# Kernel optimization log

Measured on AMD Instinct MI355X. Metric: run time of the kernel, lower is better.

The kernel has to match this reference:

```python
import jax, jax.numpy as jnp
import numpy as np

B = 65536      # batch of pose frames
FD = 267       # frame_dim
NC = 1         # num_condition_frames
NF = 1         # num_future_predictions
H = 256        # hidden_size
L = 64         # latent_size
K = 1024       # num_embeddings


def setup_inputs() -> dict:
    ks = jax.random.split(jax.random.key(0), 16)
    def W(k, o, i):
        return (jax.random.normal(k, (o, i), jnp.float32) * (1.0 / np.sqrt(i))).astype(jnp.float32)
    return {
        "x": jax.random.normal(ks[0], (B, FD * NF), jnp.float32),
        "c": jax.random.normal(ks[1], (B, FD * NC), jnp.float32),
        "fc1_w": W(ks[2], H, FD * (NF + NC)), "fc1_b": jnp.zeros((H,), jnp.float32),
        "fc2_w": W(ks[3], H, H), "fc2_b": jnp.zeros((H,), jnp.float32),
        "fc3_w": W(ks[4], H, H), "fc3_b": jnp.zeros((H,), jnp.float32),
        "mu_w": W(ks[5], L, H), "mu_b": jnp.zeros((L,), jnp.float32),
        "fc4_w": W(ks[6], H, L + FD * NC), "fc4_b": jnp.zeros((H,), jnp.float32),
        "fc5_w": W(ks[7], H, H), "fc5_b": jnp.zeros((H,), jnp.float32),
        "fc6_w": W(ks[8], H, H), "fc6_b": jnp.zeros((H,), jnp.float32),
        "out_w": W(ks[9], NF * FD, H), "out_b": jnp.zeros((NF * FD,), jnp.float32),
        "embed": jax.random.normal(ks[10], (L, K), jnp.float32),  # codebook [latent, num_embeddings]
    }


def reference(x, c, fc1_w, fc1_b, fc2_w, fc2_b, fc3_w, fc3_b, mu_w, mu_b,
              fc4_w, fc4_b, fc5_w, fc5_b, fc6_w, fc6_b, out_w, out_b, embed):
    relu = jax.nn.relu
    # encode
    s = jnp.concatenate([x, c], axis=1)                      # [B, FD*(NF+NC)]
    h = relu(s @ fc1_w.T + fc1_b)
    h = relu(h @ fc2_w.T + fc2_b)
    h = relu(h @ fc3_w.T + fc3_b)
    mu = h @ mu_w.T + mu_b                                   # [B, L]
    # vector quantizer (eval mode: no EMA buffer updates; outputs identical)
    dist = (jnp.sum(mu * mu, axis=1, keepdims=True)
            - 2.0 * (mu @ embed)
            + jnp.sum(embed * embed, axis=0, keepdims=True))  # [B, K]
    idx = jnp.argmax(-dist, axis=1)                           # [B]
    onehot = jax.nn.one_hot(idx, K, dtype=mu.dtype)           # [B, K]
    quantize = jnp.take(embed.T, idx, axis=0)                 # [B, L] codebook gather
    loss = jnp.mean((jax.lax.stop_gradient(quantize) - mu) ** 2)
    q_st = mu + jax.lax.stop_gradient(quantize - mu)          # straight-through
    avg_probs = jnp.mean(onehot, axis=0)
    perplexity = jnp.exp(-jnp.sum(avg_probs * jnp.log(avg_probs + 1e-10)))
    # decode
    s2 = jnp.concatenate([q_st, c], axis=1)                   # [B, L + FD*NC]
    h = relu(s2 @ fc4_w.T + fc4_b)
    h = relu(h @ fc5_w.T + fc5_b)
    h = relu(h @ fc6_w.T + fc6_b)
    recon = h @ out_w.T + out_b                               # [B, NF*FD]
    return recon, loss, perplexity
```

## Files before the change

kernel.cpp:

```cpp
#include <hip/hip_runtime.h>


using short8 = __attribute__((ext_vector_type(8))) short;
using f32x4  = __attribute__((ext_vector_type(4))) float;
using f32x16 = __attribute__((ext_vector_type(16))) float;

#define USHORT unsigned short
#define UINT   unsigned int

#define PS_W1  139264
#define PS_W2  65536
#define PS_MU  16384
#define PS_WE  65536

#define STRF 260
#define STRA 360
#define STRB 264

static const size_t OFF_COUNTS = 262144;
static const size_t OFF_LOSS   = 266240;
static const size_t OFF_ENORM  = 266304;
static const size_t OFF_W1     = 270400;
static const size_t OFF_W2     = 1105984;
static const size_t OFF_W3     = 1499200;
static const size_t OFF_WMU    = 1892416;
static const size_t OFF_WE     = 1990720;
static const size_t OFF_W4     = 2383936;
static const size_t OFF_W5     = 2564160;
static const size_t OFF_W6     = 2695232;
static const size_t OFF_WO     = 2826304;

__device__ __forceinline__ float b2f(USHORT u){
  return __uint_as_float(((UINT)u) << 16);
}
__device__ __forceinline__ USHORT f2b(float f){
  UINT u = __float_as_uint(f);
  u += 0x7fffu + ((u >> 16) & 1u);
  return (USHORT)(u >> 16);
}
__device__ __forceinline__ float loadF(const void* p, long i, int f32m){
  if (f32m) return ((const float*)p)[i];
  return b2f(((const USHORT*)p)[i]);
}
__device__ __forceinline__ void split3(float h, USHORT& a, USHORT& b, USHORT& c){
  a = f2b(h); float r = h - b2f(a);
  b = f2b(r); r -= b2f(b);
  c = f2b(r);
}
__device__ __forceinline__ void splitT(float h, USHORT& a, USHORT& b, USHORT& c){
  UINT u = __float_as_uint(h);
  a = (USHORT)(u >> 16);
  float r = h - __uint_as_float(u & 0xffff0000u);
  UINT v = __float_as_uint(r);
  b = (USHORT)(v >> 16);
  float r2 = r - __uint_as_float(v & 0xffff0000u);
  c = f2b(r2);
}
__device__ __forceinline__ f32x4 mfma16(short8 a, short8 b, f32x4 c){
  return __builtin_amdgcn_mfma_f32_16x16x32_bf16(a, b, c, 0, 0, 0);
}
__device__ __forceinline__ f32x16 mfma32(short8 a, short8 b, f32x16 c){
  return __builtin_amdgcn_mfma_f32_32x32x16_bf16(a, b, c, 0, 0, 0);
}
__device__ __forceinline__ void zero16(f32x16& v){
  #pragma unroll
  for (int i = 0; i < 16; ++i) v[i] = 0.f;
}
__device__ __forceinline__ void splitAT(const float* p, short8& A0, short8& A1, short8& A2){
  #pragma unroll
  for (int j = 0; j < 8; ++j){
    USHORT t0, t1, t2; splitT(p[j], t0, t1, t2);
    A0[j] = (short)t0; A1[j] = (short)t1; A2[j] = (short)t2;
  }
}
__device__ __forceinline__ int detect_f32(const void* x){
  UINT u = ((const UINT*)x)[threadIdx.x & 63];
  int e = (int)((u >> 7) & 0xFFu);
  unsigned long long m = __ballot(e >= 117 && e <= 130);
  return __popcll(m) < 32;
}

__device__ __forceinline__ void fillW(USHORT* dst, const void* src,
                                      int Kpad, int N, int Ksrc, int Nsrc,
                                      int srcStride, bool kmajor, int t,
                                      int f32m, int planes)
{
  int total = Kpad * N;
  if (t >= total) return;
  int j = t & 7, rest = t >> 3;
  int n = rest % N, kg = rest / N;
  int k = kg*8 + j;
  float v = 0.f;
  if (k < Ksrc && n < Nsrc)
    v = loadF(src, kmajor ? (long)k*srcStride + n : (long)n*srcStride + k, f32m);
  if (planes == 1){ dst[t] = f2b(v); return; }
  USHORT t0, t1, t2; split3(v, t0, t1, t2);
  dst[t] = t0; dst[total + t] = t1; dst[2*total + t] = t2;
}

__global__ void vq_prep_kernel(
    const void* xx,
    const void* fc1w, const void* fc2w, const void* fc3w,
    const void* muw,  const void* fc4w, const void* fc5w,
    const void* fc6w, const void* outw, const void* embed,
    USHORT* W1p, USHORT* W2p, USHORT* W3p, USHORT* Wmup, USHORT* Wep,
    USHORT* W4p, USHORT* W5p, USHORT* W6p, USHORT* Wop,
    float* enorm, UINT* counts, float* loss_sum)
{
  int f32m = detect_f32(xx);
  int t = blockIdx.x * 256 + threadIdx.x;
  switch (blockIdx.y){
    case 0: fillW(W1p,  fc1w, 544, 256, 534, 256, 534, false, t, f32m, 3); break;
    case 1: fillW(W2p,  fc2w, 256, 256, 256, 256, 256, false, t, f32m, 3); break;
    case 2: fillW(W3p,  fc3w, 256, 256, 256, 256, 256, false, t, f32m, 3); break;
    case 3: fillW(Wmup, muw,  256,  64, 256,  64, 256, false, t, f32m, 3); break;
    case 4: fillW(Wep,  embed, 64, 1024, 64, 1024, 1024, true, t, f32m, 3); break;
    case 5: fillW(W4p,  fc4w, 352, 256, 331, 256, 331, false, t, f32m, 1); break;
    case 6: fillW(W5p,  fc5w, 256, 256, 256, 256, 256, false, t, f32m, 1); break;
    case 7: fillW(W6p,  fc6w, 256, 256, 256, 256, 256, false, t, f32m, 1); break;
    case 8: fillW(Wop,  outw, 256, 288, 256, 267, 256, false, t, f32m, 1); break;
    case 9:
      if (t < 1024){
        double s = 0.0;
        for (int l = 0; l < 64; ++l){
          double e = (double)loadF(embed, (long)l*1024 + t, f32m); s += e*e;
        }
        enorm[t] = (float)s;
      }
      break;
    case 10:
      if (t < 1024) counts[t] = 0u;
      if (t == 1024) *loss_sum = 0.f;
      break;
  }
}

__global__ __launch_bounds__(256, 4) void vq_main_kernel(
    const void* __restrict__ x,  const void* __restrict__ cc,
    const void* __restrict__ b1, const void* __restrict__ b2,
    const void* __restrict__ b3, const void* __restrict__ bmu,
    const void* __restrict__ b4, const void* __restrict__ b5,
    const void* __restrict__ b6, const void* __restrict__ bo,
    const void* __restrict__ embed,
    const USHORT* __restrict__ W1p, const USHORT* __restrict__ W2p,
    const USHORT* __restrict__ W3p, const USHORT* __restrict__ Wmup,
    const USHORT* __restrict__ Wep, const float* __restrict__ enorm,
    const USHORT* __restrict__ W4p, const USHORT* __restrict__ W5p,
    const USHORT* __restrict__ W6p, const USHORT* __restrict__ Wop,
    UINT* __restrict__ counts, float* __restrict__ loss_sum,
    void* __restrict__ out)
{
  __shared__ __align__(16) char U[39936];
  __shared__ float rMin[4][32];
  __shared__ int   rCode[4][32];
  float*  sF = (float*)U;
  USHORT* sA = (USHORT*)U;
  USHORT* sB = (USHORT*)(U + 23040);

  const int f32m = detect_f32(x);
  const int tid  = threadIdx.x;
  const int w    = tid >> 6;
  const int lane = tid & 63;
  const int hi   = lane >> 5;
  const int nn   = lane & 31;
  const int quad = lane >> 4;
  const int l16  = lane & 15;
  const int tb0  = w * 64;
  const long gbase = (long)blockIdx.x * 32;
  const long gr    = gbase + nn;

  f32x16 acc0, acc1;
  zero16(acc0); zero16(acc1);

  for (int ks = 0; ks < 34; ++ks){
    short8 A0, A1, A2;
    if (f32m){
      #pragma unroll
      for (int j = 0; j < 8; ++j){
        int col = ks*16 + hi*8 + j;
        float v = 0.f;
        if (col < 267)      v = ((const float*)x)[gr*267 + col];
        else if (col < 534) v = ((const float*)cc)[gr*267 + (col - 267)];
        USHORT t0, t1, t2; splitT(v, t0, t1, t2);
        A0[j] = (short)t0; A1[j] = (short)t1; A2[j] = (short)t2;
      }
    } else {
      #pragma unroll
      for (int j = 0; j < 8; ++j){
        int col = ks*16 + hi*8 + j;
        USHORT u = 0;
        if (col < 267)      u = ((const USHORT*)x)[gr*267 + col];
        else if (col < 534) u = ((const USHORT*)cc)[gr*267 + (col - 267)];
        A0[j] = (short)u;
      }
    }
    const USHORT* bp = W1p + (((ks*2 + hi)*256) + tb0 + nn)*8;
    short8 B00 = *(const short8*)bp;
    short8 B01 = *(const short8*)(bp + 256);
    if (!f32m){
      acc0 = mfma32(A0, B00, acc0); acc1 = mfma32(A0, B01, acc1);
    } else {
      short8 B10 = *(const short8*)(bp + PS_W1);
      short8 B11 = *(const short8*)(bp + PS_W1 + 256);
      short8 B20 = *(const short8*)(bp + 2*PS_W1);
      short8 B21 = *(const short8*)(bp + 2*PS_W1 + 256);
      acc0 = mfma32(A0, B00, acc0); acc1 = mfma32(A0, B01, acc1);
      acc0 = mfma32(A1, B00, acc0); acc1 = mfma32(A1, B01, acc1);
      acc0 = mfma32(A2, B00, acc0); acc1 = mfma32(A2, B01, acc1);
      acc0 = mfma32(A0, B10, acc0); acc1 = mfma32(A0, B11, acc1);
      acc0 = mfma32(A1, B10, acc0); acc1 = mfma32(A1, B11, acc1);
      acc0 = mfma32(A0, B20, acc0); acc1 = mfma32(A0, B21, acc1);
    }
  }
  {
    float bs0 = loadF(b1, tb0 + nn, f32m);
    float bs1 = loadF(b1, tb0 + 32 + nn, f32m);
    #pragma unroll
    for (int reg = 0; reg < 16; ++reg){
      int r = (reg&3) + 8*(reg>>2) + 4*hi;
      sF[r*STRF + tb0 + nn]      = fmaxf(acc0[reg] + bs0, 0.f);
      sF[r*STRF + tb0 + 32 + nn] = fmaxf(acc1[reg] + bs1, 0.f);
    }
  }
  __syncthreads();

  for (int layer = 0; layer < 2; ++layer){
    const USHORT* Wp = layer ? W3p : W2p;
    const void*   bb = layer ? (const void*)b3 : (const void*)b2;
    zero16(acc0); zero16(acc1);
    #pragma unroll 2
    for (int ks = 0; ks < 16; ++ks){
      short8 A0, A1, A2;
      splitAT(&sF[nn*STRF + ks*16 + hi*8], A0, A1, A2);
      const USHORT* bp = Wp + (((ks*2 + hi)*256) + tb0 + nn)*8;
      short8 B00 = *(const short8*)bp;
      short8 B01 = *(const short8*)(bp + 256);
      acc0 = mfma32(A0, B00, acc0); acc1 = mfma32(A0, B01, acc1);
      acc0 = mfma32(A1, B00, acc0); acc1 = mfma32(A1, B01, acc1);
      acc0 = mfma32(A2, B00, acc0); acc1 = mfma32(A2, B01, acc1);
      if (f32m){
        short8 B10 = *(const short8*)(bp + PS_W2);
        short8 B11 = *(const short8*)(bp + PS_W2 + 256);
        short8 B20 = *(const short8*)(bp + 2*PS_W2);
        short8 B21 = *(const short8*)(bp + 2*PS_W2 + 256);
        acc0 = mfma32(A0, B10, acc0); acc1 = mfma32(A0, B11, acc1);
        acc0 = mfma32(A1, B10, acc0); acc1 = mfma32(A1, B11, acc1);
        acc0 = mfma32(A0, B20, acc0); acc1 = mfma32(A0, B21, acc1);
      }
    }
    __syncthreads();
    {
      float bs0 = loadF(bb, tb0 + nn, f32m);
      float bs1 = loadF(bb, tb0 + 32 + nn, f32m);
      #pragma unroll
      for (int reg = 0; reg < 16; ++reg){
        int r = (reg&3) + 8*(reg>>2) + 4*hi;
        sF[r*STRF + tb0 + nn]      = fmaxf(acc0[reg] + bs0, 0.f);
        sF[r*STRF + tb0 + 32 + nn] = fmaxf(acc1[reg] + bs1, 0.f);
      }
    }
    __syncthreads();
  }

  {
    f32x4 am0, am1;
    #pragma unroll
    for (int i = 0; i < 4; ++i){ am0[i] = 0.f; am1[i] = 0.f; }
    #pragma unroll 2
    for (int kc = 0; kc < 8; ++kc){
      short8 A0a, A1a, A2a, A0b, A1b, A2b;
      splitAT(&sF[l16*STRF + kc*32 + quad*8],        A0a, A1a, A2a);
      splitAT(&sF[(l16 + 16)*STRF + kc*32 + quad*8], A0b, A1b, A2b);
      const USHORT* bp = Wmup + ((kc*4 + quad)*64 + w*16 + l16)*8;
      short8 Bm0 = *(const short8*)bp;
      am0 = mfma16(A0a, Bm0, am0); am1 = mfma16(A0b, Bm0, am1);
      am0 = mfma16(A1a, Bm0, am0); am1 = mfma16(A1b, Bm0, am1);
      am0 = mfma16(A2a, Bm0, am0); am1 = mfma16(A2b, Bm0, am1);
      if (f32m){
        short8 Bm1 = *(const short8*)(bp + PS_MU);
        am0 = mfma16(A0a, Bm1, am0); am1 = mfma16(A0b, Bm1, am1);
        am0 = mfma16(A1a, Bm1, am0); am1 = mfma16(A1b, Bm1, am1);
        short8 Bm2 = *(const short8*)(bp + 2*PS_MU);
        am0 = mfma16(A0a, Bm2, am0); am1 = mfma16(A0b, Bm2, am1);
      }
    }
    __syncthreads();
    float bm = loadF(bmu, w*16 + l16, f32m);
    #pragma unroll
    for (int r = 0; r < 4; ++r){
      sF[(quad*4 + r)*STRF + w*16 + l16]        = am0[r] + bm;
      sF[(quad*4 + r + 16)*STRF + w*16 + l16]   = am1[r] + bm;
    }
    __syncthreads();
  }

  {
    short8 MA0[4], MA1[4], MA2[4];
    #pragma unroll
    for (int ks = 0; ks < 4; ++ks)
      splitAT(&sF[nn*STRF + ks*16 + hi*8], MA0[ks], MA1[ks], MA2[ks]);
    float minv[16]; int minc[16];
    #pragma unroll
    for (int i = 0; i < 16; ++i){ minv[i] = 3.4e38f; minc[i] = 0; }
    for (int tt = 0; tt < 8; ++tt){
      int cb = w*256 + tt*32;
      f32x16 ad; zero16(ad);
      #pragma unroll
      for (int ks = 0; ks < 4; ++ks){
        const USHORT* bp = Wep + (((ks*2 + hi)*1024) + cb + nn)*8;
        short8 B0 = *(const short8*)bp;
        ad = mfma32(MA0[ks], B0, ad);
        ad = mfma32(MA1[ks], B0, ad);
        ad = mfma32(MA2[ks], B0, ad);
        if (f32m){
          short8 B1 = *(const short8*)(bp + PS_WE);
          ad = mfma32(MA0[ks], B1, ad);
          ad = mfma32(MA1[ks], B1, ad);
          short8 B2 = *(const short8*)(bp + 2*PS_WE);
          ad = mfma32(MA0[ks], B2, ad);
        }
      }
      int code = cb + nn;
      float en = enorm[code];
      #pragma unroll
      for (int reg = 0; reg < 16; ++reg){
        float d = en - 2.f*ad[reg];
        if (d < minv[reg] || (d == minv[reg] && code < minc[reg])){ minv[reg] = d; minc[reg] = code; }
      }
    }
    #pragma unroll
    for (int off = 16; off >= 1; off >>= 1){
      #pragma unroll
      for (int reg = 0; reg < 16; ++reg){
        float ov = __shfl_xor(minv[reg], off, 64);
        int   oc = __shfl_xor(minc[reg], off, 64);
        if (ov < minv[reg] || (ov == minv[reg] && oc < minc[reg])){ minv[reg] = ov; minc[reg] = oc; }
      }
    }
    if (nn == 0){
      #pragma unroll
      for (int reg = 0; reg < 16; ++reg){
        int r = (reg&3) + 8*(reg>>2) + 4*hi;
        rMin[w][r]  = minv[reg];
        rCode[w][r] = minc[reg];
      }
    }
  }
  __syncthreads();

  if (tid < 32){
    float bv = rMin[0][tid]; int bc = rCode[0][tid];
    #pragma unroll
    for (int ww = 1; ww < 4; ++ww){
      float v = rMin[ww][tid]; int cd = rCode[ww][tid];
      if (v < bv || (v == bv && cd < bc)){ bv = v; bc = cd; }
    }
    rCode[0][tid] = bc;
    atomicAdd(&counts[bc], 1u);
  }
  __syncthreads();

  {
    int lrow = tid >> 3;
    int j0 = (tid & 7) * 8;
    int code = rCode[0][lrow];
    float lp = 0.f;
    #pragma unroll
    for (int jj = 0; jj < 8; ++jj){
      int l = j0 + jj;
      float qv = loadF(embed, (long)l*1024 + code, f32m);
      float d = qv - sF[lrow*STRF + l];
      lp += d*d;
    }
    #pragma unroll
    for (int off = 32; off >= 1; off >>= 1) lp += __shfl_xor(lp, off, 64);
    if (lane == 0) rMin[0][w] = lp;
  }
  __syncthreads();
  if (tid == 0)
    atomicAdd(loss_sum, rMin[0][0] + rMin[0][1] + rMin[0][2] + rMin[0][3]);

  {
    int rr = tid >> 3, jg = tid & 7;
    int code = rCode[0][rr];
    short8 qv = *(const short8*)(Wep + ((long)jg*1024 + code)*8);
    *(short8*)&sA[rr*STRA + jg*8] = qv;
  }
  for (int rr = w*8; rr < w*8 + 8; ++rr){
    long grow = gbase + rr;
    for (int col = 64 + lane; col < 360; col += 64){
      float v = (col < 331) ? loadF(cc, grow*267 + (col - 64), f32m) : 0.f;
      sA[rr*STRA + col] = f2b(v);
    }
  }
  __syncthreads();

  zero16(acc0); zero16(acc1);
  #pragma unroll 2
  for (int ks = 0; ks < 22; ++ks){
    short8 A = *(const short8*)&sA[nn*STRA + ks*16 + hi*8];
    const USHORT* bp = W4p + (((ks*2 + hi)*256) + tb0 + nn)*8;
    acc0 = mfma32(A, *(const short8*)bp,         acc0);
    acc1 = mfma32(A, *(const short8*)(bp + 256), acc1);
  }
  {
    float bs0 = loadF(b4, tb0 + nn, f32m);
    float bs1 = loadF(b4, tb0 + 32 + nn, f32m);
    #pragma unroll
    for (int reg = 0; reg < 16; ++reg){
      int r = (reg&3) + 8*(reg>>2) + 4*hi;
      sB[r*STRB + tb0 + nn]      = f2b(fmaxf(acc0[reg] + bs0, 0.f));
      sB[r*STRB + tb0 + 32 + nn] = f2b(fmaxf(acc1[reg] + bs1, 0.f));
    }
  }
  __syncthreads();

  zero16(acc0); zero16(acc1);
  #pragma unroll 4
  for (int ks = 0; ks < 16; ++ks){
    short8 A = *(const short8*)&sB[nn*STRB + ks*16 + hi*8];
    const USHORT* bp = W5p + (((ks*2 + hi)*256) + tb0 + nn)*8;
    acc0 = mfma32(A, *(const short8*)bp,         acc0);
    acc1 = mfma32(A, *(const short8*)(bp + 256), acc1);
  }
  __syncthreads();
  {
    float bs0 = loadF(b5, tb0 + nn, f32m);
    float bs1 = loadF(b5, tb0 + 32 + nn, f32m);
    #pragma unroll
    for (int reg = 0; reg < 16; ++reg){
      int r = (reg&3) + 8*(reg>>2) + 4*hi;
      sA[r*STRA + tb0 + nn]      = f2b(fmaxf(acc0[reg] + bs0, 0.f));
      sA[r*STRA + tb0 + 32 + nn] = f2b(fmaxf(acc1[reg] + bs1, 0.f));
    }
  }
  __syncthreads();

  zero16(acc0); zero16(acc1);
  #pragma unroll 4
  for (int ks = 0; ks < 16; ++ks){
    short8 A = *(const short8*)&sA[nn*STRA + ks*16 + hi*8];
    const USHORT* bp = W6p + (((ks*2 + hi)*256) + tb0 + nn)*8;
    acc0 = mfma32(A, *(const short8*)bp,         acc0);
    acc1 = mfma32(A, *(const short8*)(bp + 256), acc1);
  }
  __syncthreads();
  {
    float bs0 = loadF(b6, tb0 + nn, f32m);
    float bs1 = loadF(b6, tb0 + 32 + nn, f32m);
    #pragma unroll
    for (int reg = 0; reg < 16; ++reg){
      int r = (reg&3) + 8*(reg>>2) + 4*hi;
      sB[r*STRB + tb0 + nn]      = f2b(fmaxf(acc0[reg] + bs0, 0.f));
      sB[r*STRB + tb0 + 32 + nn] = f2b(fmaxf(acc1[reg] + bs1, 0.f));
    }
  }
  __syncthreads();

  {
    f32x16 acco0, acco1, acco2;
    zero16(acco0); zero16(acco1); zero16(acco2);
    #pragma unroll 2
    for (int ks = 0; ks < 16; ++ks){
      short8 A = *(const short8*)&sB[nn*STRB + ks*16 + hi*8];
      const USHORT* bp = Wop + (((ks*2 + hi)*288) + w*64 + nn)*8;
      acco0 = mfma32(A, *(const short8*)bp,         acco0);
      acco1 = mfma32(A, *(const short8*)(bp + 256), acco1);
      if (w == 3) acco2 = mfma32(A, *(const short8*)(bp + 512), acco2);
    }
    int ntiles = (w == 3) ? 3 : 2;
    #pragma unroll
    for (int t = 0; t < 3; ++t){
      if (t < ntiles){
        int col = w*64 + t*32 + nn;
        if (col < 267){
          float bias = loadF(bo, col, f32m);
          f32x16& a = (t == 0) ? acco0 : (t == 1) ? acco1 : acco2;
          #pragma unroll
          for (int reg = 0; reg < 16; ++reg){
            int r = (reg&3) + 8*(reg>>2) + 4*hi;
            long oi = (gbase + r)*267 + col;
            float val = a[reg] + bias;
            if (f32m) ((float*)out)[oi] = val;
            else      ((USHORT*)out)[oi] = f2b(val);
          }
        }
      }
    }
  }
}

__global__ void vq_fin_kernel(const void* __restrict__ x,
                              const UINT* __restrict__ counts,
                              const float* __restrict__ loss_sum,
                              void* __restrict__ out)
{
  __shared__ float red[4];
  int f32m = detect_f32(x);
  int tid = threadIdx.x;
  float Hl = 0.f;
  for (int k = tid; k < 1024; k += 256){
    float p = (float)counts[k] * (1.f/65536.f);
    Hl -= p * logf(p + 1e-10f);
  }
  #pragma unroll
  for (int off = 32; off >= 1; off >>= 1) Hl += __shfl_xor(Hl, off, 64);
  if ((tid & 63) == 0) red[tid >> 6] = Hl;
  __syncthreads();
  if (tid == 0){
    float H = red[0] + red[1] + red[2] + red[3];
    float loss = *loss_sum * (1.f/4194304.f);
    float ppx  = expf(H);
    size_t base = (size_t)65536*267;
    if (f32m){
      ((float*)out)[base]     = loss;
      ((float*)out)[base + 1] = ppx;
    } else {
      ((USHORT*)out)[base]     = f2b(loss);
      ((USHORT*)out)[base + 1] = f2b(ppx);
    }
  }
}

extern "C" void kernel_launch(void* const* d_in, const int* in_sizes, int n_in,
                              void* d_out, int out_size, void* d_ws, size_t ws_size,
                              hipStream_t stream)
{
  const void* x    = d_in[0];
  const void* c    = d_in[1];
  const void* fc1w = d_in[2];
  const void* fc1b = d_in[3];
  const void* fc2w = d_in[4];
  const void* fc2b = d_in[5];
  const void* fc3w = d_in[6];
  const void* fc3b = d_in[7];
  const void* muw  = d_in[8];
  const void* mub  = d_in[9];
  const void* fc4w = d_in[10];
  const void* fc4b = d_in[11];
  const void* fc5w = d_in[12];
  const void* fc5b = d_in[13];
  const void* fc6w = d_in[14];
  const void* fc6b = d_in[15];
  const void* outw = d_in[16];
  const void* outb = d_in[17];
  const void* embed= d_in[18];

  char* ws = (char*)d_ws;
  UINT*   counts = (UINT*)  (ws + OFF_COUNTS);
  float*  lsum   = (float*) (ws + OFF_LOSS);
  float*  enorm  = (float*) (ws + OFF_ENORM);
  USHORT* W1p = (USHORT*)(ws + OFF_W1);
  USHORT* W2p = (USHORT*)(ws + OFF_W2);
  USHORT* W3p = (USHORT*)(ws + OFF_W3);
  USHORT* Wmup= (USHORT*)(ws + OFF_WMU);
  USHORT* Wep = (USHORT*)(ws + OFF_WE);
  USHORT* W4p = (USHORT*)(ws + OFF_W4);
  USHORT* W5p = (USHORT*)(ws + OFF_W5);
  USHORT* W6p = (USHORT*)(ws + OFF_W6);
  USHORT* Wop = (USHORT*)(ws + OFF_WO);

  dim3 pgrid(544, 11, 1);
  vq_prep_kernel<<<pgrid, 256, 0, stream>>>(
      x, fc1w, fc2w, fc3w, muw, fc4w, fc5w, fc6w, outw, embed,
      W1p, W2p, W3p, Wmup, Wep, W4p, W5p, W6p, Wop, enorm, counts, lsum);

  vq_main_kernel<<<2048, 256, 0, stream>>>(
      x, c, fc1b, fc2b, fc3b, mub, fc4b, fc5b, fc6b, outb, embed,
      W1p, W2p, W3p, Wmup, Wep, enorm,
      W4p, W5p, W6p, Wop, counts, lsum, d_out);

  vq_fin_kernel<<<1, 256, 0, stream>>>(x, counts, lsum, d_out);
}
```

Measured before the change: 1.180 ms.

## Retile main kernel to 64-row blocks with 8 waves and register-prefetched weights

```diff
diff --git a/kernel.cpp b/kernel.cpp
--- a/kernel.cpp
+++ b/kernel.cpp
@@ -135,7 +135,7 @@
   }
 }
 
-__global__ __launch_bounds__(256, 4) void vq_main_kernel(
+__global__ __launch_bounds__(512, 4) void vq_main_kernel(
     const void* __restrict__ x,  const void* __restrict__ cc,
     const void* __restrict__ b1, const void* __restrict__ b2,
     const void* __restrict__ b3, const void* __restrict__ bmu,
@@ -150,12 +150,14 @@
     UINT* __restrict__ counts, float* __restrict__ loss_sum,
     void* __restrict__ out)
 {
-  __shared__ __align__(16) char U[39936];
-  __shared__ float rMin[4][32];
-  __shared__ int   rCode[4][32];
+  __shared__ __align__(16) char U[79872];
+  __shared__ int   codes[64];
+  __shared__ float lossRed[8];
   float*  sF = (float*)U;
   USHORT* sA = (USHORT*)U;
-  USHORT* sB = (USHORT*)(U + 23040);
+  USHORT* sB = (USHORT*)(U + 46080);
+  float*  pMin  = (float*)(U + 66560);
+  int*    pCode = (int*)  (U + 68608);
 
   const int f32m = detect_f32(x);
   const int tid  = threadIdx.x;
@@ -165,61 +167,83 @@
   const int nn   = lane & 31;
   const int quad = lane >> 4;
   const int l16  = lane & 15;
-  const int tb0  = w * 64;
-  const long gbase = (long)blockIdx.x * 32;
-  const long gr    = gbase + nn;
+  const int tb0  = w * 32;
+  const long gbase = (long)blockIdx.x * 64;
 
   f32x16 acc0, acc1;
   zero16(acc0); zero16(acc1);
 
-  for (int ks = 0; ks < 34; ++ks){
-    short8 A0, A1, A2;
-    if (f32m){
+  if (f32m){
+    float ca0[8], ca1[8], na0[8], na1[8];
+    auto loadA8 = [&](int ks, float* a0, float* a1){
       #pragma unroll
       for (int j = 0; j < 8; ++j){
         int col = ks*16 + hi*8 + j;
-        float v = 0.f;
-        if (col < 267)      v = ((const float*)x)[gr*267 + col];
-        else if (col < 534) v = ((const float*)cc)[gr*267 + (col - 267)];
-        USHORT t0, t1, t2; splitT(v, t0, t1, t2);
-        A0[j] = (short)t0; A1[j] = (short)t1; A2[j] = (short)t2;
-      }
-    } else {
+        float v0 = 0.f, v1 = 0.f;
+        if (col < 267){
+          v0 = ((const float*)x)[(gbase + nn)*267 + col];
+          v1 = ((const float*)x)[(gbase + nn + 32)*267 + col];
+        } else if (col < 534){
+          v0 = ((const float*)cc)[(gbase + nn)*267 + (col - 267)];
+          v1 = ((const float*)cc)[(gbase + nn + 32)*267 + (col - 267)];
+        }
+        a0[j] = v0; a1[j] = v1;
+      }
+    };
+    auto fc1body = [&](const float* a0, const float* a1, int ks){
+      short8 A00, A01, A02, A10, A11, A12;
+      #pragma unroll
+      for (int j = 0; j < 8; ++j){
+        USHORT t0, t1, t2;
+        splitT(a0[j], t0, t1, t2); A00[j]=(short)t0; A01[j]=(short)t1; A02[j]=(short)t2;
+        splitT(a1[j], t0, t1, t2); A10[j]=(short)t0; A11[j]=(short)t1; A12[j]=(short)t2;
+      }
+      const USHORT* bp = W1p + (((ks*2 + hi)*256) + tb0 + nn)*8;
+      short8 B0 = *(const short8*)bp;
+      short8 B1 = *(const short8*)(bp + PS_W1);
+      short8 B2 = *(const short8*)(bp + 2*PS_W1);
+      acc0 = mfma32(A00, B0, acc0); acc1 = mfma32(A10, B0, acc1);
+      acc0 = mfma32(A01, B0, acc0); acc1 = mfma32(A11, B0, acc1);
+      acc0 = mfma32(A02, B0, acc0); acc1 = mfma32(A12, B0, acc1);
+      acc0 = mfma32(A00, B1, acc0); acc1 = mfma32(A10, B1, acc1);
+      acc0 = mfma32(A01, B1, acc0); acc1 = mfma32(A11, B1, acc1);
+      acc0 = mfma32(A00, B2, acc0); acc1 = mfma32(A10, B2, acc1);
+    };
+    loadA8(0, ca0, ca1);
+    for (int ks = 0; ks < 34; ks += 2){
+      loadA8(ks + 1, na0, na1);
+      fc1body(ca0, ca1, ks);
+      if (ks + 2 < 34) loadA8(ks + 2, ca0, ca1);
+      fc1body(na0, na1, ks + 1);
+    }
+  } else {
+    for (int ks = 0; ks < 34; ++ks){
+      short8 A0a, A0b;
       #pragma unroll
       for (int j = 0; j < 8; ++j){
         int col = ks*16 + hi*8 + j;
-        USHORT u = 0;
-        if (col < 267)      u = ((const USHORT*)x)[gr*267 + col];
-        else if (col < 534) u = ((const USHORT*)cc)[gr*267 + (col - 267)];
-        A0[j] = (short)u;
-      }
-    }
-    const USHORT* bp = W1p + (((ks*2 + hi)*256) + tb0 + nn)*8;
-    short8 B00 = *(const short8*)bp;
-    short8 B01 = *(const short8*)(bp + 256);
-    if (!f32m){
-      acc0 = mfma32(A0, B00, acc0); acc1 = mfma32(A0, B01, acc1);
-    } else {
-      short8 B10 = *(const short8*)(bp + PS_W1);
-      short8 B11 = *(const short8*)(bp + PS_W1 + 256);
-      short8 B20 = *(const short8*)(bp + 2*PS_W1);
-      short8 B21 = *(const short8*)(bp + 2*PS_W1 + 256);
-      acc0 = mfma32(A0, B00, acc0); acc1 = mfma32(A0, B01, acc1);
-      acc0 = mfma32(A1, B00, acc0); acc1 = mfma32(A1, B01, acc1);
-      acc0 = mfma32(A2, B00, acc0); acc1 = mfma32(A2, B01, acc1);
-      acc0 = mfma32(A0, B10, acc0); acc1 = mfma32(A0, B11, acc1);
-      acc0 = mfma32(A1, B10, acc0); acc1 = mfma32(A1, B11, acc1);
-      acc0 = mfma32(A0, B20, acc0); acc1 = mfma32(A0, B21, acc1);
-    }
-  }
-  {
-    float bs0 = loadF(b1, tb0 + nn, f32m);
-    float bs1 = loadF(b1, tb0 + 32 + nn, f32m);
+        USHORT u0 = 0, u1 = 0;
+        if (col < 267){
+          u0 = ((const USHORT*)x)[(gbase + nn)*267 + col];
+          u1 = ((const USHORT*)x)[(gbase + nn + 32)*267 + col];
+        } else if (col < 534){
+          u0 = ((const USHORT*)cc)[(gbase + nn)*267 + (col - 267)];
+          u1 = ((const USHORT*)cc)[(gbase + nn + 32)*267 + (col - 267)];
+        }
+        A0a[j] = (short)u0; A0b[j] = (short)u1;
+      }
+      const USHORT* bp = W1p + (((ks*2 + hi)*256) + tb0 + nn)*8;
+      short8 B0 = *(const short8*)bp;
+      acc0 = mfma32(A0a, B0, acc0); acc1 = mfma32(A0b, B0, acc1);
+    }
+  }
+  {
+    float bs = loadF(b1, tb0 + nn, f32m);
     #pragma unroll
     for (int reg = 0; reg < 16; ++reg){
       int r = (reg&3) + 8*(reg>>2) + 4*hi;
-      sF[r*STRF + tb0 + nn]      = fmaxf(acc0[reg] + bs0, 0.f);
-      sF[r*STRF + tb0 + 32 + nn] = fmaxf(acc1[reg] + bs1, 0.f);
+      sF[(long)r*STRF + tb0 + nn]        = fmaxf(acc0[reg] + bs, 0.f);
+      sF[(long)(r+32)*STRF + tb0 + nn]   = fmaxf(acc1[reg] + bs, 0.f);
     }
   }
   __syncthreads();
@@ -228,82 +252,91 @@
     const USHORT* Wp = layer ? W3p : W2p;
     const void*   bb = layer ? (const void*)b3 : (const void*)b2;
     zero16(acc0); zero16(acc1);
-    #pragma unroll 2
-    for (int ks = 0; ks < 16; ++ks){
-      short8 A0, A1, A2;
-      splitAT(&sF[nn*STRF + ks*16 + hi*8], A0, A1, A2);
+    short8 Bc0, Bc1, Bc2, Bn0, Bn1, Bn2;
+    auto loadB3 = [&](int ks, short8& o0, short8& o1, short8& o2){
       const USHORT* bp = Wp + (((ks*2 + hi)*256) + tb0 + nn)*8;
-      short8 B00 = *(const short8*)bp;
-      short8 B01 = *(const short8*)(bp + 256);
-      acc0 = mfma32(A0, B00, acc0); acc1 = mfma32(A0, B01, acc1);
-      acc0 = mfma32(A1, B00, acc0); acc1 = mfma32(A1, B01, acc1);
-      acc0 = mfma32(A2, B00, acc0); acc1 = mfma32(A2, B01, acc1);
+      o0 = *(const short8*)bp;
+      o1 = *(const short8*)(bp + PS_W2);
+      o2 = *(const short8*)(bp + 2*PS_W2);
+    };
+    auto body = [&](int ks, short8 b0p, short8 b1p, short8 b2p){
+      short8 A00, A01, A02, A10, A11, A12;
+      splitAT(&sF[(long)nn*STRF + ks*16 + hi*8],        A00, A01, A02);
+      splitAT(&sF[(long)(nn + 32)*STRF + ks*16 + hi*8], A10, A11, A12);
+      acc0 = mfma32(A00, b0p, acc0); acc1 = mfma32(A10, b0p, acc1);
+      acc0 = mfma32(A01, b0p, acc0); acc1 = mfma32(A11, b0p, acc1);
+      acc0 = mfma32(A02, b0p, acc0); acc1 = mfma32(A12, b0p, acc1);
       if (f32m){
-        short8 B10 = *(const short8*)(bp + PS_W2);
-        short8 B11 = *(const short8*)(bp + PS_W2 + 256);
-        short8 B20 = *(const short8*)(bp + 2*PS_W2);
-        short8 B21 = *(const short8*)(bp + 2*PS_W2 + 256);
-        acc0 = mfma32(A0, B10, acc0); acc1 = mfma32(A0, B11, acc1);
-        acc0 = mfma32(A1, B10, acc0); acc1 = mfma32(A1, B11, acc1);
-        acc0 = mfma32(A0, B20, acc0); acc1 = mfma32(A0, B21, acc1);
-      }
+        acc0 = mfma32(A00, b1p, acc0); acc1 = mfma32(A10, b1p, acc1);
+        acc0 = mfma32(A01, b1p, acc0); acc1 = mfma32(A11, b1p, acc1);
+        acc0 = mfma32(A00, b2p, acc0); acc1 = mfma32(A10, b2p, acc1);
+      }
+    };
+    loadB3(0, Bc0, Bc1, Bc2);
+    for (int ks = 0; ks < 16; ks += 2){
+      loadB3(ks + 1, Bn0, Bn1, Bn2);
+      body(ks, Bc0, Bc1, Bc2);
+      if (ks + 2 < 16) loadB3(ks + 2, Bc0, Bc1, Bc2);
+      body(ks + 1, Bn0, Bn1, Bn2);
     }
     __syncthreads();
     {
-      float bs0 = loadF(bb, tb0 + nn, f32m);
-      float bs1 = loadF(bb, tb0 + 32 + nn, f32m);
+      float bs = loadF(bb, tb0 + nn, f32m);
       #pragma unroll
       for (int reg = 0; reg < 16; ++reg){
         int r = (reg&3) + 8*(reg>>2) + 4*hi;
-        sF[r*STRF + tb0 + nn]      = fmaxf(acc0[reg] + bs0, 0.f);
-        sF[r*STRF + tb0 + 32 + nn] = fmaxf(acc1[reg] + bs1, 0.f);
+        sF[(long)r*STRF + tb0 + nn]      = fmaxf(acc0[reg] + bs, 0.f);
+        sF[(long)(r+32)*STRF + tb0 + nn] = fmaxf(acc1[reg] + bs, 0.f);
       }
     }
     __syncthreads();
   }
 
   {
+    const int rg = w >> 2;
+    const int mcol = (w & 3) * 16;
     f32x4 am0, am1;
     #pragma unroll
     for (int i = 0; i < 4; ++i){ am0[i] = 0.f; am1[i] = 0.f; }
     #pragma unroll 2
     for (int kc = 0; kc < 8; ++kc){
-      short8 A0a, A1a, A2a, A0b, A1b, A2b;
-      splitAT(&sF[l16*STRF + kc*32 + quad*8],        A0a, A1a, A2a);
-      splitAT(&sF[(l16 + 16)*STRF + kc*32 + quad*8], A0b, A1b, A2b);
-      const USHORT* bp = Wmup + ((kc*4 + quad)*64 + w*16 + l16)*8;
+      short8 Aa0, Aa1, Aa2, Ab0, Ab1, Ab2;
+      splitAT(&sF[(long)(rg*32 + l16)*STRF + kc*32 + quad*8],      Aa0, Aa1, Aa2);
+      splitAT(&sF[(long)(rg*32 + 16 + l16)*STRF + kc*32 + quad*8], Ab0, Ab1, Ab2);
+      const USHORT* bp = Wmup + ((kc*4 + quad)*64 + mcol + l16)*8;
       short8 Bm0 = *(const short8*)bp;
-      am0 = mfma16(A0a, Bm0, am0); am1 = mfma16(A0b, Bm0, am1);
-      am0 = mfma16(A1a, Bm0, am0); am1 = mfma16(A1b, Bm0, am1);
-      am0 = mfma16(A2a, Bm0, am0); am1 = mfma16(A2b, Bm0, am1);
+      am0 = mfma16(Aa0, Bm0, am0); am1 = mfma16(Ab0, Bm0, am1);
+      am0 = mfma16(Aa1, Bm0, am0); am1 = mfma16(Ab1, Bm0, am1);
+      am0 = mfma16(Aa2, Bm0, am0); am1 = mfma16(Ab2, Bm0, am1);
       if (f32m){
         short8 Bm1 = *(const short8*)(bp + PS_MU);
-        am0 = mfma16(A0a, Bm1, am0); am1 = mfma16(A0b, Bm1, am1);
-        am0 = mfma16(A1a, Bm1, am0); am1 = mfma16(A1b, Bm1, am1);
+        am0 = mfma16(Aa0, Bm1, am0); am1 = mfma16(Ab0, Bm1, am1);
+        am0 = mfma16(Aa1, Bm1, am0); am1 = mfma16(Ab1, Bm1, am1);
         short8 Bm2 = *(const short8*)(bp + 2*PS_MU);
-        am0 = mfma16(A0a, Bm2, am0); am1 = mfma16(A0b, Bm2, am1);
+        am0 = mfma16(Aa0, Bm2, am0); am1 = mfma16(Ab0, Bm2, am1);
       }
     }
     __syncthreads();
-    float bm = loadF(bmu, w*16 + l16, f32m);
+    float bm = loadF(bmu, mcol + l16, f32m);
     #pragma unroll
     for (int r = 0; r < 4; ++r){
-      sF[(quad*4 + r)*STRF + w*16 + l16]        = am0[r] + bm;
-      sF[(quad*4 + r + 16)*STRF + w*16 + l16]   = am1[r] + bm;
+      sF[(long)(rg*32 + quad*4 + r)*STRF + mcol + l16]      = am0[r] + bm;
+      sF[(long)(rg*32 + 16 + quad*4 + r)*STRF + mcol + l16] = am1[r] + bm;
     }
     __syncthreads();
   }
 
-  {
+  for (int rt = 0; rt < 2; ++rt){
     short8 MA0[4], MA1[4], MA2[4];
     #pragma unroll
     for (int ks = 0; ks < 4; ++ks)
-      splitAT(&sF[nn*STRF + ks*16 + hi*8], MA0[ks], MA1[ks], MA2[ks]);
+      splitAT(&sF[(long)(rt*32 + nn)*STRF + ks*16 + hi*8], MA0[ks], MA1[ks], MA2[ks]);
     float minv[16]; int minc[16];
     #pragma unroll
     for (int i = 0; i < 16; ++i){ minv[i] = 3.4e38f; minc[i] = 0; }
-    for (int tt = 0; tt < 8; ++tt){
-      int cb = w*256 + tt*32;
+    #pragma unroll 1
+    for (int tt = 0; tt < 4; ++tt){
+      int cb = w*128 + tt*32;
       f32x16 ad; zero16(ad);
       #pragma unroll
       for (int ks = 0; ks < 4; ++ks){
@@ -340,22 +373,22 @@
     if (nn == 0){
       #pragma unroll
       for (int reg = 0; reg < 16; ++reg){
-        int r = (reg&3) + 8*(reg>>2) + 4*hi;
-        rMin[w][r]  = minv[reg];
-        rCode[w][r] = minc[reg];
-      }
-    }
-  }
-  __syncthreads();
-
-  if (tid < 32){
-    float bv = rMin[0][tid]; int bc = rCode[0][tid];
-    #pragma unroll
-    for (int ww = 1; ww < 4; ++ww){
-      float v = rMin[ww][tid]; int cd = rCode[ww][tid];
+        int r = (reg&3) + 8*(reg>>2) + 4*hi + rt*32;
+        pMin[w*64 + r]  = minv[reg];
+        pCode[w*64 + r] = minc[reg];
+      }
+    }
+  }
+  __syncthreads();
+
+  if (tid < 64){
+    float bv = pMin[tid]; int bc = pCode[tid];
+    #pragma unroll
+    for (int ww = 1; ww < 8; ++ww){
+      float v = pMin[ww*64 + tid]; int cd = pCode[ww*64 + tid];
       if (v < bv || (v == bv && cd < bc)){ bv = v; bc = cd; }
     }
-    rCode[0][tid] = bc;
+    codes[tid] = bc;
     atomicAdd(&counts[bc], 1u);
   }
   __syncthreads();
@@ -363,32 +396,35 @@
   {
     int lrow = tid >> 3;
     int j0 = (tid & 7) * 8;
-    int code = rCode[0][lrow];
+    int code = codes[lrow];
     float lp = 0.f;
     #pragma unroll
     for (int jj = 0; jj < 8; ++jj){
       int l = j0 + jj;
       float qv = loadF(embed, (long)l*1024 + code, f32m);
-      float d = qv - sF[lrow*STRF + l];
+      float d = qv - sF[(long)lrow*STRF + l];
       lp += d*d;
     }
     #pragma unroll
     for (int off = 32; off >= 1; off >>= 1) lp += __shfl_xor(lp, off, 64);
-    if (lane == 0) rMin[0][w] = lp;
-  }
-  __syncthreads();
-  if (tid == 0)
-    atomicAdd(loss_sum, rMin[0][0] + rMin[0][1] + rMin[0][2] + rMin[0][3]);
+    if (lane == 0) lossRed[w] = lp;
+  }
+  __syncthreads();
+  if (tid == 0){
+    float s = 0.f;
+    #pragma unroll
+    for (int ww = 0; ww < 8; ++ww) s += lossRed[ww];
+    atomicAdd(loss_sum, s);
+  }
 
   {
     int rr = tid >> 3, jg = tid & 7;
-    int code = rCode[0][rr];
-    short8 qv = *(const short8*)(Wep + ((long)jg*1024 + code)*8);
-    *(short8*)&sA[rr*STRA + jg*8] = qv;
+    int code = codes[rr];
+    *(short8*)&sA[rr*STRA + jg*8] = *(const short8*)(Wep + ((long)jg*1024 + code)*8);
   }
   for (int rr = w*8; rr < w*8 + 8; ++rr){
     long grow = gbase + rr;
-    for (int col = 64 + lane; col < 360; col += 64){
+    for (int col = 64 + lane; col < STRA; col += 64){
       float v = (col < 331) ? loadF(cc, grow*267 + (col - 64), f32m) : 0.f;
       sA[rr*STRA + col] = f2b(v);
     }
@@ -396,95 +432,135 @@
   __syncthreads();
 
   zero16(acc0); zero16(acc1);
-  #pragma unroll 2
-  for (int ks = 0; ks < 22; ++ks){
-    short8 A = *(const short8*)&sA[nn*STRA + ks*16 + hi*8];
-    const USHORT* bp = W4p + (((ks*2 + hi)*256) + tb0 + nn)*8;
-    acc0 = mfma32(A, *(const short8*)bp,         acc0);
-    acc1 = mfma32(A, *(const short8*)(bp + 256), acc1);
-  }
-  {
-    float bs0 = loadF(b4, tb0 + nn, f32m);
-    float bs1 = loadF(b4, tb0 + 32 + nn, f32m);
+  #pragma unroll
+  for (int ch = 0; ch < 2; ++ch){
+    short8 Bk[11];
+    #pragma unroll
+    for (int i = 0; i < 11; ++i){
+      int ks = ch*11 + i;
+      Bk[i] = *(const short8*)(W4p + (((ks*2 + hi)*256) + tb0 + nn)*8);
+    }
+    #pragma unroll
+    for (int i = 0; i < 11; ++i){
+      int ks = ch*11 + i;
+      short8 A0 = *(const short8*)&sA[nn*STRA + ks*16 + hi*8];
+      short8 A1 = *(const short8*)&sA[(nn + 32)*STRA + ks*16 + hi*8];
+      acc0 = mfma32(A0, Bk[i], acc0);
+      acc1 = mfma32(A1, Bk[i], acc1);
+    }
+  }
+  {
+    float bs = loadF(b4, tb0 + nn, f32m);
     #pragma unroll
     for (int reg = 0; reg < 16; ++reg){
       int r = (reg&3) + 8*(reg>>2) + 4*hi;
-      sB[r*STRB + tb0 + nn]      = f2b(fmaxf(acc0[reg] + bs0, 0.f));
-      sB[r*STRB + tb0 + 32 + nn] = f2b(fmaxf(acc1[reg] + bs1, 0.f));
+      sB[r*STRB + tb0 + nn]        = f2b(fmaxf(acc0[reg] + bs, 0.f));
+      sB[(r+32)*STRB + tb0 + nn]   = f2b(fmaxf(acc1[reg] + bs, 0.f));
     }
   }
   __syncthreads();
 
   zero16(acc0); zero16(acc1);
-  #pragma unroll 4
-  for (int ks = 0; ks < 16; ++ks){
-    short8 A = *(const short8*)&sB[nn*STRB + ks*16 + hi*8];
-    const USHORT* bp = W5p + (((ks*2 + hi)*256) + tb0 + nn)*8;
-    acc0 = mfma32(A, *(const short8*)bp,         acc0);
-    acc1 = mfma32(A, *(const short8*)(bp + 256), acc1);
-  }
-  __syncthreads();
-  {
-    float bs0 = loadF(b5, tb0 + nn, f32m);
-    float bs1 = loadF(b5, tb0 + 32 + nn, f32m);
+  {
+    short8 Bk[16];
+    #pragma unroll
+    for (int i = 0; i < 16; ++i)
+      Bk[i] = *(const short8*)(W5p + (((i*2 + hi)*256) + tb0 + nn)*8);
+    #pragma unroll
+    for (int i = 0; i < 16; ++i){
+      short8 A0 = *(const short8*)&sB[nn*STRB + i*16 + hi*8];
+      short8 A1 = *(const short8*)&sB[(nn + 32)*STRB + i*16 + hi*8];
+      acc0 = mfma32(A0, Bk[i], acc0);
+      acc1 = mfma32(A1, Bk[i], acc1);
+    }
+  }
+  __syncthreads();
+  {
+    float bs = loadF(b5, tb0 + nn, f32m);
     #pragma unroll
     for (int reg = 0; reg < 16; ++reg){
       int r = (reg&3) + 8*(reg>>2) + 4*hi;
-      sA[r*STRA + tb0 + nn]      = f2b(fmaxf(acc0[reg] + bs0, 0.f));
-      sA[r*STRA + tb0 + 32 + nn] = f2b(fmaxf(acc1[reg] + bs1, 0.f));
+      sA[r*STRA + tb0 + nn]        = f2b(fmaxf(acc0[reg] + bs, 0.f));
+      sA[(r+32)*STRA + tb0 + nn]   = f2b(fmaxf(acc1[reg] + bs, 0.f));
     }
   }
   __syncthreads();
 
   zero16(acc0); zero16(acc1);
-  #pragma unroll 4
-  for (int ks = 0; ks < 16; ++ks){
-    short8 A = *(const short8*)&sA[nn*STRA + ks*16 + hi*8];
-    const USHORT* bp = W6p + (((ks*2 + hi)*256) + tb0 + nn)*8;
-    acc0 = mfma32(A, *(const short8*)bp,         acc0);
-    acc1 = mfma32(A, *(const short8*)(bp + 256), acc1);
-  }
-  __syncthreads();
-  {
-    float bs0 = loadF(b6, tb0 + nn, f32m);
-    float bs1 = loadF(b6, tb0 + 32 + nn, f32m);
+  {
+    short8 Bk[16];
+    #pragma unroll
+    for (int i = 0; i < 16; ++i)
+      Bk[i] = *(const short8*)(W6p + (((i*2 + hi)*256) + tb0 + nn)*8);
+    #pragma unroll
+    for (int i = 0; i < 16; ++i){
+      short8 A0 = *(const short8*)&sA[nn*STRA + i*16 + hi*8];
+      short8 A1 = *(const short8*)&sA[(nn + 32)*STRA + i*16 + hi*8];
+      acc0 = mfma32(A0, Bk[i], acc0);
+      acc1 = mfma32(A1, Bk[i], acc1);
+    }
+  }
+  __syncthreads();
+  {
+    float bs = loadF(b6, tb0 + nn, f32m);
     #pragma unroll
     for (int reg = 0; reg < 16; ++reg){
       int r = (reg&3) + 8*(reg>>2) + 4*hi;
-      sB[r*STRB + tb0 + nn]      = f2b(fmaxf(acc0[reg] + bs0, 0.f));
-      sB[r*STRB + tb0 + 32 + nn] = f2b(fmaxf(acc1[reg] + bs1, 0.f));
-    }
-  }
-  __syncthreads();
-
-  {
-    f32x16 acco0, acco1, acco2;
-    zero16(acco0); zero16(acco1); zero16(acco2);
-    #pragma unroll 2
-    for (int ks = 0; ks < 16; ++ks){
-      short8 A = *(const short8*)&sB[nn*STRB + ks*16 + hi*8];
-      const USHORT* bp = Wop + (((ks*2 + hi)*288) + w*64 + nn)*8;
-      acco0 = mfma32(A, *(const short8*)bp,         acco0);
-      acco1 = mfma32(A, *(const short8*)(bp + 256), acco1);
-      if (w == 3) acco2 = mfma32(A, *(const short8*)(bp + 512), acco2);
-    }
-    int ntiles = (w == 3) ? 3 : 2;
-    #pragma unroll
-    for (int t = 0; t < 3; ++t){
-      if (t < ntiles){
-        int col = w*64 + t*32 + nn;
-        if (col < 267){
-          float bias = loadF(bo, col, f32m);
-          f32x16& a = (t == 0) ? acco0 : (t == 1) ? acco1 : acco2;
-          #pragma unroll
-          for (int reg = 0; reg < 16; ++reg){
-            int r = (reg&3) + 8*(reg>>2) + 4*hi;
-            long oi = (gbase + r)*267 + col;
-            float val = a[reg] + bias;
-            if (f32m) ((float*)out)[oi] = val;
-            else      ((USHORT*)out)[oi] = f2b(val);
-          }
-        }
+      sB[r*STRB + tb0 + nn]        = f2b(fmaxf(acc0[reg] + bs, 0.f));
+      sB[(r+32)*STRB + tb0 + nn]   = f2b(fmaxf(acc1[reg] + bs, 0.f));
+    }
+  }
+  __syncthreads();
+
+  {
+    short8 Bk[16];
+    #pragma unroll
+    for (int i = 0; i < 16; ++i)
+      Bk[i] = *(const short8*)(Wop + (((i*2 + hi)*288) + w*32 + nn)*8);
+    f32x16 o0, o1; zero16(o0); zero16(o1);
+    #pragma unroll
+    for (int i = 0; i < 16; ++i){
+      short8 A0 = *(const short8*)&sB[nn*STRB + i*16 + hi*8];
+      short8 A1 = *(const short8*)&sB[(nn + 32)*STRB + i*16 + hi*8];
+      o0 = mfma32(A0, Bk[i], o0);
+      o1 = mfma32(A1, Bk[i], o1);
+    }
+    int col = w*32 + nn;
+    float bias = loadF(bo, col, f32m);
+    #pragma unroll
+    for (int reg = 0; reg < 16; ++reg){
+      int r = (reg&3) + 8*(reg>>2) + 4*hi;
+      long oi0 = (gbase + r)*267 + col;
+      long oi1 = (gbase + r + 32)*267 + col;
+      float v0 = o0[reg] + bias, v1 = o1[reg] + bias;
+      if (f32m){ ((float*)out)[oi0] = v0; ((float*)out)[oi1] = v1; }
+      else     { ((USHORT*)out)[oi0] = f2b(v0); ((USHORT*)out)[oi1] = f2b(v1); }
+    }
+  }
+  if (w == 7){
+    short8 Bk[16];
+    #pragma unroll
+    for (int i = 0; i < 16; ++i)
+      Bk[i] = *(const short8*)(Wop + (((i*2 + hi)*288) + 256 + nn)*8);
+    f32x16 o0, o1; zero16(o0); zero16(o1);
+    #pragma unroll
+    for (int i = 0; i < 16; ++i){
+      short8 A0 = *(const short8*)&sB[nn*STRB + i*16 + hi*8];
+      short8 A1 = *(const short8*)&sB[(nn + 32)*STRB + i*16 + hi*8];
+      o0 = mfma32(A0, Bk[i], o0);
+      o1 = mfma32(A1, Bk[i], o1);
+    }
+    int col = 256 + nn;
+    if (col < 267){
+      float bias = loadF(bo, col, f32m);
+      #pragma unroll
+      for (int reg = 0; reg < 16; ++reg){
+        int r = (reg&3) + 8*(reg>>2) + 4*hi;
+        long oi0 = (gbase + r)*267 + col;
+        long oi1 = (gbase + r + 32)*267 + col;
+        float v0 = o0[reg] + bias, v1 = o1[reg] + bias;
+        if (f32m){ ((float*)out)[oi0] = v0; ((float*)out)[oi1] = v1; }
+        else     { ((USHORT*)out)[oi0] = f2b(v0); ((USHORT*)out)[oi1] = f2b(v1); }
       }
     }
   }
@@ -565,7 +641,7 @@
       x, fc1w, fc2w, fc3w, muw, fc4w, fc5w, fc6w, outw, embed,
       W1p, W2p, W3p, Wmup, Wep, W4p, W5p, W6p, Wop, enorm, counts, lsum);
 
-  vq_main_kernel<<<2048, 256, 0, stream>>>(
+  vq_main_kernel<<<1024, 512, 0, stream>>>(
       x, c, fc1b, fc2b, fc3b, mub, fc4b, fc5b, fc6b, outb, embed,
       W1p, W2p, W3p, Wmup, Wep, enorm,
       W4p, W5p, W6p, Wop, counts, lsum, d_out);
```

Result: slower. 1.324 ms (+12.2%).

## Store activations in LDS as pre-split bf16 triple planes instead of fp32

Applied to the files above, without the earlier changes.

```diff
diff --git a/kernel.cpp b/kernel.cpp
--- a/kernel.cpp
+++ b/kernel.cpp
@@ -13,7 +13,7 @@
 #define PS_MU  16384
 #define PS_WE  65536
 
-#define STRF 260
+#define STRT 264
 #define STRA 360
 #define STRB 264
 
@@ -65,13 +65,6 @@
 __device__ __forceinline__ void zero16(f32x16& v){
   #pragma unroll
   for (int i = 0; i < 16; ++i) v[i] = 0.f;
-}
-__device__ __forceinline__ void splitAT(const float* p, short8& A0, short8& A1, short8& A2){
-  #pragma unroll
-  for (int j = 0; j < 8; ++j){
-    USHORT t0, t1, t2; splitT(p[j], t0, t1, t2);
-    A0[j] = (short)t0; A1[j] = (short)t1; A2[j] = (short)t2;
-  }
 }
 __device__ __forceinline__ int detect_f32(const void* x){
   UINT u = ((const UINT*)x)[threadIdx.x & 63];
@@ -135,7 +128,7 @@
   }
 }
 
-__global__ __launch_bounds__(256, 4) void vq_main_kernel(
+__global__ __launch_bounds__(256, 3) void vq_main_kernel(
     const void* __restrict__ x,  const void* __restrict__ cc,
     const void* __restrict__ b1, const void* __restrict__ b2,
     const void* __restrict__ b3, const void* __restrict__ bmu,
@@ -150,12 +143,14 @@
     UINT* __restrict__ counts, float* __restrict__ loss_sum,
     void* __restrict__ out)
 {
-  __shared__ __align__(16) char U[39936];
+  __shared__ __align__(16) char U[50688];
   __shared__ float rMin[4][32];
   __shared__ int   rCode[4][32];
-  float*  sF = (float*)U;
-  USHORT* sA = (USHORT*)U;
-  USHORT* sB = (USHORT*)(U + 23040);
+  USHORT* sT0 = (USHORT*)U;
+  USHORT* sT1 = (USHORT*)(U + 16896);
+  USHORT* sT2 = (USHORT*)(U + 33792);
+  USHORT* sA  = (USHORT*)U;
+  USHORT* sB  = (USHORT*)(U + 23040);
 
   const int f32m = detect_f32(x);
   const int tid  = threadIdx.x;
@@ -218,8 +213,13 @@
     #pragma unroll
     for (int reg = 0; reg < 16; ++reg){
       int r = (reg&3) + 8*(reg>>2) + 4*hi;
-      sF[r*STRF + tb0 + nn]      = fmaxf(acc0[reg] + bs0, 0.f);
-      sF[r*STRF + tb0 + 32 + nn] = fmaxf(acc1[reg] + bs1, 0.f);
+      float h0 = fmaxf(acc0[reg] + bs0, 0.f);
+      float h1 = fmaxf(acc1[reg] + bs1, 0.f);
+      USHORT t0,t1,t2;
+      splitT(h0, t0,t1,t2);
+      sT0[r*STRT + tb0 + nn] = t0; sT1[r*STRT + tb0 + nn] = t1; sT2[r*STRT + tb0 + nn] = t2;
+      splitT(h1, t0,t1,t2);
+      sT0[r*STRT + tb0 + 32 + nn] = t0; sT1[r*STRT + tb0 + 32 + nn] = t1; sT2[r*STRT + tb0 + 32 + nn] = t2;
     }
   }
   __syncthreads();
@@ -230,8 +230,10 @@
     zero16(acc0); zero16(acc1);
     #pragma unroll 2
     for (int ks = 0; ks < 16; ++ks){
-      short8 A0, A1, A2;
-      splitAT(&sF[nn*STRF + ks*16 + hi*8], A0, A1, A2);
+      const int ao = nn*STRT + ks*16 + hi*8;
+      short8 A0 = *(const short8*)&sT0[ao];
+      short8 A1 = *(const short8*)&sT1[ao];
+      short8 A2 = *(const short8*)&sT2[ao];
       const USHORT* bp = Wp + (((ks*2 + hi)*256) + tb0 + nn)*8;
       short8 B00 = *(const short8*)bp;
       short8 B01 = *(const short8*)(bp + 256);
@@ -255,8 +257,13 @@
       #pragma unroll
       for (int reg = 0; reg < 16; ++reg){
         int r = (reg&3) + 8*(reg>>2) + 4*hi;
-        sF[r*STRF + tb0 + nn]      = fmaxf(acc0[reg] + bs0, 0.f);
-        sF[r*STRF + tb0 + 32 + nn] = fmaxf(acc1[reg] + bs1, 0.f);
+        float h0 = fmaxf(acc0[reg] + bs0, 0.f);
+        float h1 = fmaxf(acc1[reg] + bs1, 0.f);
+        USHORT t0,t1,t2;
+        splitT(h0, t0,t1,t2);
+        sT0[r*STRT + tb0 + nn] = t0; sT1[r*STRT + tb0 + nn] = t1; sT2[r*STRT + tb0 + nn] = t2;
+        splitT(h1, t0,t1,t2);
+        sT0[r*STRT + tb0 + 32 + nn] = t0; sT1[r*STRT + tb0 + 32 + nn] = t1; sT2[r*STRT + tb0 + 32 + nn] = t2;
       }
     }
     __syncthreads();
@@ -268,28 +275,42 @@
     for (int i = 0; i < 4; ++i){ am0[i] = 0.f; am1[i] = 0.f; }
     #pragma unroll 2
     for (int kc = 0; kc < 8; ++kc){
-      short8 A0a, A1a, A2a, A0b, A1b, A2b;
-      splitAT(&sF[l16*STRF + kc*32 + quad*8],        A0a, A1a, A2a);
-      splitAT(&sF[(l16 + 16)*STRF + kc*32 + quad*8], A0b, A1b, A2b);
+      const int aoa = l16*STRT + kc*32 + quad*8;
+      const int aob = (l16 + 16)*STRT + kc*32 + quad*8;
+      short8 Aa0 = *(const short8*)&sT0[aoa];
+      short8 Aa1 = *(const short8*)&sT1[aoa];
+      short8 Aa2 = *(const short8*)&sT2[aoa];
+      short8 Ab0 = *(const short8*)&sT0[aob];
+      short8 Ab1 = *(const short8*)&sT1[aob];
+      short8 Ab2 = *(const short8*)&sT2[aob];
       const USHORT* bp = Wmup + ((kc*4 + quad)*64 + w*16 + l16)*8;
       short8 Bm0 = *(const short8*)bp;
-      am0 = mfma16(A0a, Bm0, am0); am1 = mfma16(A0b, Bm0, am1);
-      am0 = mfma16(A1a, Bm0, am0); am1 = mfma16(A1b, Bm0, am1);
-      am0 = mfma16(A2a, Bm0, am0); am1 = mfma16(A2b, Bm0, am1);
+      am0 = mfma16(Aa0, Bm0, am0); am1 = mfma16(Ab0, Bm0, am1);
+      am0 = mfma16(Aa1, Bm0, am0); am1 = mfma16(Ab1, Bm0, am1);
+      am0 = mfma16(Aa2, Bm0, am0); am1 = mfma16(Ab2, Bm0, am1);
       if (f32m){
         short8 Bm1 = *(const short8*)(bp + PS_MU);
-        am0 = mfma16(A0a, Bm1, am0); am1 = mfma16(A0b, Bm1, am1);
-        am0 = mfma16(A1a, Bm1, am0); am1 = mfma16(A1b, Bm1, am1);
+        am0 = mfma16(Aa0, Bm1, am0); am1 = mfma16(Ab0, Bm1, am1);
+        am0 = mfma16(Aa1, Bm1, am0); am1 = mfma16(Ab1, Bm1, am1);
         short8 Bm2 = *(const short8*)(bp + 2*PS_MU);
-        am0 = mfma16(A0a, Bm2, am0); am1 = mfma16(A0b, Bm2, am1);
+        am0 = mfma16(Aa0, Bm2, am0); am1 = mfma16(Ab0, Bm2, am1);
       }
     }
     __syncthreads();
     float bm = loadF(bmu, w*16 + l16, f32m);
     #pragma unroll
     for (int r = 0; r < 4; ++r){
-      sF[(quad*4 + r)*STRF + w*16 + l16]        = am0[r] + bm;
-      sF[(quad*4 + r + 16)*STRF + w*16 + l16]   = am1[r] + bm;
+      float m0 = am0[r] + bm;
+      float m1 = am1[r] + bm;
+      USHORT t0,t1,t2;
+      splitT(m0, t0,t1,t2);
+      sT0[(quad*4 + r)*STRT + w*16 + l16] = t0;
+      sT1[(quad*4 + r)*STRT + w*16 + l16] = t1;
+      sT2[(quad*4 + r)*STRT + w*16 + l16] = t2;
+      splitT(m1, t0,t1,t2);
+      sT0[(quad*4 + r + 16)*STRT + w*16 + l16] = t0;
+      sT1[(quad*4 + r + 16)*STRT + w*16 + l16] = t1;
+      sT2[(quad*4 + r + 16)*STRT + w*16 + l16] = t2;
     }
     __syncthreads();
   }
@@ -297,8 +318,12 @@
   {
     short8 MA0[4], MA1[4], MA2[4];
     #pragma unroll
-    for (int ks = 0; ks < 4; ++ks)
-      splitAT(&sF[nn*STRF + ks*16 + hi*8], MA0[ks], MA1[ks], MA2[ks]);
+    for (int ks = 0; ks < 4; ++ks){
+      const int ao = nn*STRT + ks*16 + hi*8;
+      MA0[ks] = *(const short8*)&sT0[ao];
+      MA1[ks] = *(const short8*)&sT1[ao];
+      MA2[ks] = *(const short8*)&sT2[ao];
+    }
     float minv[16]; int minc[16];
     #pragma unroll
     for (int i = 0; i < 16; ++i){ minv[i] = 3.4e38f; minc[i] = 0; }
@@ -369,7 +394,8 @@
     for (int jj = 0; jj < 8; ++jj){
       int l = j0 + jj;
       float qv = loadF(embed, (long)l*1024 + code, f32m);
-      float d = qv - sF[lrow*STRF + l];
+      float muf = b2f(sT0[lrow*STRT + l]) + b2f(sT1[lrow*STRT + l]) + b2f(sT2[lrow*STRT + l]);
+      float d = qv - muf;
       lp += d*d;
     }
     #pragma unroll
```

After: 1.217 ms. +3.1%, slower.
